# Performance work log

Measured on AMD Instinct MI355X. Metric: run time of the kernel, lower is better.

## Reference

```python
import jax, jax.numpy as jnp
import numpy as np

T, B, V, D, H = 1024, 128, 50257, 128, 512


def _lstm_cell(x, h, c, w_ih, w_hh, b_ih, b_hh):
    # x: [B, D], h/c: [B, H]; gates: [B, 4H] in PyTorch i,f,g,o order
    gates = x @ w_ih.T + h @ w_hh.T + b_ih + b_hh
    i, f, g, o = jnp.split(gates, 4, axis=-1)
    c_new = jax.nn.sigmoid(f) * c + jax.nn.sigmoid(i) * jnp.tanh(g)
    h_new = jax.nn.sigmoid(o) * jnp.tanh(c_new)
    return h_new, c_new


def setup_inputs() -> dict:
    key = jax.random.key(0)
    ks = jax.random.split(key, 7)
    s = 1.0 / np.sqrt(H)
    return {
        "input_ids": jax.random.randint(ks[0], (T, B), 0, V),
        "seq_len": jnp.sort(jax.random.randint(ks[1], (B,), 0, T)),
        "emb_weight": jax.random.normal(ks[2], (V, D), jnp.float32) * 0.1,
        "w_ih": jax.random.uniform(ks[3], (4 * H, D), jnp.float32, -s, s),
        "w_hh": jax.random.uniform(ks[4], (4 * H, H), jnp.float32, -s, s),
        "b_ih": jax.random.uniform(ks[5], (4 * H,), jnp.float32, -s, s),
        "b_hh": jax.random.uniform(ks[6], (4 * H,), jnp.float32, -s, s),
    }


def reference(input_ids, seq_len, emb_weight, w_ih, w_hh, b_ih, b_hh):
    Tn, Bn = input_ids.shape
    Hn = w_hh.shape[1]
    dt = emb_weight.dtype
    z = jnp.zeros((Bn, Hn), dt)

    def step(carry, inp):
        h, c, last_h, last_c = carry
        t, ids = inp
        x = emb_weight[ids]                       # embedding lookup (dropout=identity, eval)
        h_new, c_new = _lstm_cell(x, h, c, w_ih, w_hh, b_ih, b_hh)
        # hold previously reported features once timestep >= seq_len (skip blend at t==0)
        hold = ((t > 0) & (t >= seq_len)).astype(dt)[:, None]
        blend_c = c_new * (1.0 - hold) + last_c * hold
        blend_h = h_new * (1.0 - hold) + last_h * hold
        # RNN internal state keeps evolving (module is stateful across steps)
        return (h_new, c_new, blend_h, blend_c), None

    (_, _, _, final_c), _ = jax.lax.scan(
        step, (z, z, z, z), (jnp.arange(Tn), input_ids)
    )
    return final_c  # [B, H] mask-blended last cell state
```

## Files before the change

kernel.cpp:

```cpp
#include <hip/hip_runtime.h>

typedef _Float16 half8 __attribute__((ext_vector_type(8)));
typedef float float4v __attribute__((ext_vector_type(4)));
typedef unsigned long long u64;

#define TSEQ  1024
#define BATCH 128
#define HID   512
#define DIN   128

#define HW_STRIDE 264
#define HBUF_WORDS (8 * HW_STRIDE)
#define GOFF (2 * HBUF_WORDS * 4)
#define LDS_BYTES (GOFF + 4 * 8 * 32 * 4)

#define WS_H16_OFF  0
#define WS_BAR_OFF  (2 * BATCH * HID * 2)
#define WS_XALL_OFF (1u << 20)
#define WS_NEED     ((size_t)WS_XALL_OFF + (size_t)TSEQ * BATCH * DIN * 2)

__device__ inline half8 cvt8(float4v a, float4v b) {
    half8 r;
    r[0] = (_Float16)a[0]; r[1] = (_Float16)a[1];
    r[2] = (_Float16)a[2]; r[3] = (_Float16)a[3];
    r[4] = (_Float16)b[0]; r[5] = (_Float16)b[1];
    r[6] = (_Float16)b[2]; r[7] = (_Float16)b[3];
    return r;
}

__device__ inline float sigm(float x) {
    return __builtin_amdgcn_rcpf(1.0f + __builtin_amdgcn_exp2f(-1.44269504f * x));
}
__device__ inline float tanh_fast(float x) { return 2.0f * sigm(2.0f * x) - 1.0f; }

template <bool XA>
__global__ __launch_bounds__(256, 1)
void lstm_persistent(const int* __restrict__ ids,
                     const int* __restrict__ seq_len,
                     const float* __restrict__ emb,
                     const float* __restrict__ w_ih,
                     const float* __restrict__ w_hh,
                     const float* __restrict__ b_ih,
                     const float* __restrict__ b_hh,
                     float* __restrict__ out,
                     _Float16* __restrict__ h16,
                     _Float16* __restrict__ x_all,
                     int* __restrict__ bar)
{
    __shared__ __align__(16) char smem[LDS_BYTES];
    unsigned* hsu = (unsigned*)smem;
    _Float16* hsh = (_Float16*)smem;
    float*    gs  = (float*)(smem + GOFF);

    const int tid  = threadIdx.x;
    const int lane = tid & 63;
    const int wv   = tid >> 6;
    const int team = blockIdx.x & 15;
    const int p    = blockIdx.x >> 4;
    const int rowbase   = team * 8;
    const int unit_base = p * 32 + wv * 8;

    const int col  = lane & 15;
    const int kq   = lane >> 4;
    const int arow = lane & 7;
    const int my_row  = lane >> 3;
    const int my_unit = unit_base + (lane & 7);

    if (XA) {
        for (int pair = blockIdx.x * 256 + tid; pair < TSEQ * BATCH;
             pair += 256 * 256) {
            const float* src = emb + (size_t)ids[pair] * DIN;
            _Float16* dst = x_all + (size_t)pair * DIN;
#pragma unroll
            for (int k = 0; k < 16; ++k) {
                float4v a = *(const float4v*)(src + k * 8);
                float4v c = *(const float4v*)(src + k * 8 + 4);
                *(half8*)(dst + k * 8) = cvt8(a, c);
            }
        }
        __threadfence();
        __syncthreads();
        if (tid == 0) {
            __hip_atomic_fetch_add(bar, 1, __ATOMIC_RELEASE,
                                   __HIP_MEMORY_SCOPE_AGENT);
            int g = 0;
            while (__hip_atomic_load(bar, __ATOMIC_ACQUIRE,
                                     __HIP_MEMORY_SCOPE_AGENT) < 256
                   && ++g < (1 << 26)) { }
        }
        __syncthreads();
        __threadfence();
    }

    int tmax = 0, my_tstar = 0;
    for (int r = 0; r < 8; ++r) {
        int s  = seq_len[rowbase + r];
        int ts = (s > 0) ? (s - 1) : 0;
        if (r == my_row) my_tstar = ts;
        tmax = (ts > tmax) ? ts : tmax;
    }

    const int wrow0 = (col & 3) * HID + unit_base + (col >> 2);
    const int wrow1 = (col & 3) * HID + unit_base + 4 + (col >> 2);
    const float bias0 = b_ih[wrow0] + b_hh[wrow0];
    const float bias1 = b_ih[wrow1] + b_hh[wrow1];

    half8 whhf0[16], whhf1[16];
#pragma unroll
    for (int kt = 0; kt < 16; ++kt) {
        const float* s0 = w_hh + (size_t)wrow0 * HID + kt * 32 + kq * 8;
        const float* s1 = w_hh + (size_t)wrow1 * HID + kt * 32 + kq * 8;
        whhf0[kt] = cvt8(*(const float4v*)s0, *(const float4v*)(s0 + 4));
        whhf1[kt] = cvt8(*(const float4v*)s1, *(const float4v*)(s1 + 4));
    }
    half8 wihf0[4], wihf1[4];
#pragma unroll
    for (int kt = 0; kt < 4; ++kt) {
        const float* s0 = w_ih + (size_t)wrow0 * DIN + kt * 32 + kq * 8;
        const float* s1 = w_ih + (size_t)wrow1 * DIN + kt * 32 + kq * 8;
        wihf0[kt] = cvt8(*(const float4v*)s0, *(const float4v*)(s0 + 4));
        wihf1[kt] = cvt8(*(const float4v*)s1, *(const float4v*)(s1 + 4));
    }

    float c_state = 0.0f;
    const int crow = tid >> 5;
    const int coff = tid & 31;

    half8 xf[4], xn[4];
    if (XA) {
        const _Float16* x0 = x_all + ((size_t)0 * BATCH + rowbase + arow) * DIN;
        const int t1 = (tmax > 0) ? 1 : 0;
        const _Float16* x1 = x_all + ((size_t)t1 * BATCH + rowbase + arow) * DIN;
#pragma unroll
        for (int kt = 0; kt < 4; ++kt) {
            xf[kt] = *(const half8*)(x0 + kt * 32 + kq * 8);
            xn[kt] = *(const half8*)(x1 + kt * 32 + kq * 8);
        }
    } else {
        const int id0 = ids[rowbase + arow];
        const float* xrow = emb + (size_t)id0 * DIN;
#pragma unroll
        for (int kt = 0; kt < 4; ++kt) {
            const float* s = xrow + kt * 32 + kq * 8;
            xf[kt] = cvt8(*(const float4v*)s, *(const float4v*)(s + 4));
        }
    }

    float4v a0 = {bias0, bias0, bias0, bias0}, b0 = {0,0,0,0}, c0 = {0,0,0,0}, d0 = {0,0,0,0};
    float4v a1 = {bias1, bias1, bias1, bias1}, b1 = {0,0,0,0}, c1 = {0,0,0,0}, d1 = {0,0,0,0};
    a0 = __builtin_amdgcn_mfma_f32_16x16x32_f16(xf[0], wihf0[0], a0, 0, 0, 0);
    b0 = __builtin_amdgcn_mfma_f32_16x16x32_f16(xf[1], wihf0[1], b0, 0, 0, 0);
    c0 = __builtin_amdgcn_mfma_f32_16x16x32_f16(xf[2], wihf0[2], c0, 0, 0, 0);
    d0 = __builtin_amdgcn_mfma_f32_16x16x32_f16(xf[3], wihf0[3], d0, 0, 0, 0);
    a1 = __builtin_amdgcn_mfma_f32_16x16x32_f16(xf[0], wihf1[0], a1, 0, 0, 0);
    b1 = __builtin_amdgcn_mfma_f32_16x16x32_f16(xf[1], wihf1[1], b1, 0, 0, 0);
    c1 = __builtin_amdgcn_mfma_f32_16x16x32_f16(xf[2], wihf1[2], c1, 0, 0, 0);
    d1 = __builtin_amdgcn_mfma_f32_16x16x32_f16(xf[3], wihf1[3], d1, 0, 0, 0);

    const u64 LSBM = 0x0001000100010001ull;

    for (int t = 0; t <= tmax; ++t) {
        const int bs = t & 1;
        int id_next = 0;
        if (!XA) {
            const int tn = (t < tmax) ? (t + 1) : t;
            id_next = ids[tn * BATCH + rowbase + arow];
        }

        if (t > 0) {
            const u64* rowp = (const u64*)(h16
                + (size_t)((t + 1) & 1) * BATCH * HID + (rowbase + crow) * HID);
            const u64 want = ((((t - 1) >> 1) & 1) ^ 1) ? LSBM : 0ull;
            unsigned* dstw = hsu + bs * HBUF_WORDS + crow * HW_STRIDE + 2 * coff;
            u64 v[4];
            unsigned pending = 0xF;
#pragma unroll
            for (int j = 0; j < 4; ++j)
                v[j] = __hip_atomic_load(rowp + coff + 32 * j,
                                         __ATOMIC_RELAXED, __HIP_MEMORY_SCOPE_AGENT);
#pragma unroll
            for (int j = 0; j < 4; ++j) {
                if (((v[j] ^ want) & LSBM) == 0) {
                    *(u64*)(dstw + 64 * j) = v[j];
                    pending &= ~(1u << j);
                }
            }
            int round = 0, guard = 0;
            while (pending) {
#pragma unroll
                for (int j = 0; j < 4; ++j) {
                    if (pending & (1u << j)) {
                        u64 x = __hip_atomic_load(rowp + coff + 32 * j,
                                                  __ATOMIC_RELAXED,
                                                  __HIP_MEMORY_SCOPE_AGENT);
                        if (((x ^ want) & LSBM) == 0) {
                            *(u64*)(dstw + 64 * j) = x;
                            pending &= ~(1u << j);
                        }
                    }
                }
                if (!pending) break;
                if (++round >= 3) __builtin_amdgcn_s_sleep(1);
                if (++guard > (1 << 20)) break;
            }
        }
        __syncthreads();

        float4v xraw[8];
        if (!XA) {
            const float* xrow = emb + (size_t)id_next * DIN;
#pragma unroll
            for (int kt = 0; kt < 4; ++kt) {
                xraw[2 * kt]     = *(const float4v*)(xrow + kt * 32 + kq * 8);
                xraw[2 * kt + 1] = *(const float4v*)(xrow + kt * 32 + kq * 8 + 4);
            }
        }

        if (t > 0) {
            const _Float16* hb = hsh + bs * HBUF_WORDS * 2;
#pragma unroll
            for (int kt = 0; kt < 16; ++kt) {
                half8 af = *(const half8*)(hb + arow * (HW_STRIDE * 2) + kt * 32 + kq * 8);
                switch (kt & 3) {
                case 0:
                    a0 = __builtin_amdgcn_mfma_f32_16x16x32_f16(af, whhf0[kt], a0, 0, 0, 0);
                    a1 = __builtin_amdgcn_mfma_f32_16x16x32_f16(af, whhf1[kt], a1, 0, 0, 0);
                    break;
                case 1:
                    b0 = __builtin_amdgcn_mfma_f32_16x16x32_f16(af, whhf0[kt], b0, 0, 0, 0);
                    b1 = __builtin_amdgcn_mfma_f32_16x16x32_f16(af, whhf1[kt], b1, 0, 0, 0);
                    break;
                case 2:
                    c0 = __builtin_amdgcn_mfma_f32_16x16x32_f16(af, whhf0[kt], c0, 0, 0, 0);
                    c1 = __builtin_amdgcn_mfma_f32_16x16x32_f16(af, whhf1[kt], c1, 0, 0, 0);
                    break;
                default:
                    d0 = __builtin_amdgcn_mfma_f32_16x16x32_f16(af, whhf0[kt], d0, 0, 0, 0);
                    d1 = __builtin_amdgcn_mfma_f32_16x16x32_f16(af, whhf1[kt], d1, 0, 0, 0);
                }
            }
        }
        const float4v g0 = (a0 + b0) + (c0 + d0);
        const float4v g1 = (a1 + b1) + (c1 + d1);

        float* gw = gs + wv * 256;
        if (lane < 32) {
            const int grow = (lane >> 4) * 4;
#pragma unroll
            for (int r = 0; r < 4; ++r) {
                gw[(grow + r) * 32 + col]      = g0[r];
                gw[(grow + r) * 32 + 16 + col] = g1[r];
            }
        }
        const float4v g4 = *(const float4v*)(gw + my_row * 32 + (lane & 7) * 4);

        const float i_s = sigm(g4[0]);
        const float f_s = sigm(g4[1]);
        const float g_t = tanh_fast(g4[2]);
        const float o_s = sigm(g4[3]);
        c_state = f_s * c_state + i_s * g_t;
        const float hn = o_s * tanh_fast(c_state);

        if (t == my_tstar)
            out[(rowbase + my_row) * HID + my_unit] = c_state;

        {
            const unsigned pub_phase = (((unsigned)t >> 1) & 1u) ^ 1u;
            unsigned short hb16 = __builtin_bit_cast(unsigned short, (_Float16)hn);
            hb16 = (unsigned short)((hb16 & 0xFFFEu) | pub_phase);
            __hip_atomic_store((unsigned short*)h16
                                   + (size_t)(t & 1) * BATCH * HID
                                   + (rowbase + my_row) * HID + my_unit,
                               hb16, __ATOMIC_RELAXED, __HIP_MEMORY_SCOPE_AGENT);
        }

        if (XA) {
#pragma unroll
            for (int kt = 0; kt < 4; ++kt) xf[kt] = xn[kt];
            const int t2 = (t + 2 <= tmax) ? (t + 2) : tmax;
            const _Float16* xs2 = x_all + ((size_t)t2 * BATCH + rowbase + arow) * DIN;
#pragma unroll
            for (int kt = 0; kt < 4; ++kt)
                xn[kt] = *(const half8*)(xs2 + kt * 32 + kq * 8);
        } else {
#pragma unroll
            for (int kt = 0; kt < 4; ++kt)
                xf[kt] = cvt8(xraw[2 * kt], xraw[2 * kt + 1]);
        }

        a0 = (float4v){bias0, bias0, bias0, bias0}; b0 = (float4v){0,0,0,0};
        c0 = (float4v){0,0,0,0};                    d0 = (float4v){0,0,0,0};
        a1 = (float4v){bias1, bias1, bias1, bias1}; b1 = (float4v){0,0,0,0};
        c1 = (float4v){0,0,0,0};                    d1 = (float4v){0,0,0,0};
        a0 = __builtin_amdgcn_mfma_f32_16x16x32_f16(xf[0], wihf0[0], a0, 0, 0, 0);
        b0 = __builtin_amdgcn_mfma_f32_16x16x32_f16(xf[1], wihf0[1], b0, 0, 0, 0);
        c0 = __builtin_amdgcn_mfma_f32_16x16x32_f16(xf[2], wihf0[2], c0, 0, 0, 0);
        d0 = __builtin_amdgcn_mfma_f32_16x16x32_f16(xf[3], wihf0[3], d0, 0, 0, 0);
        a1 = __builtin_amdgcn_mfma_f32_16x16x32_f16(xf[0], wihf1[0], a1, 0, 0, 0);
        b1 = __builtin_amdgcn_mfma_f32_16x16x32_f16(xf[1], wihf1[1], b1, 0, 0, 0);
        c1 = __builtin_amdgcn_mfma_f32_16x16x32_f16(xf[2], wihf1[2], c1, 0, 0, 0);
        d1 = __builtin_amdgcn_mfma_f32_16x16x32_f16(xf[3], wihf1[3], d1, 0, 0, 0);
    }
}

extern "C" void kernel_launch(void* const* d_in, const int* in_sizes, int n_in,
                              void* d_out, int out_size, void* d_ws, size_t ws_size,
                              hipStream_t stream)
{
    const int*   ids  = (const int*)d_in[0];
    const int*   slen = (const int*)d_in[1];
    const float* emb  = (const float*)d_in[2];
    const float* wih  = (const float*)d_in[3];
    const float* whh  = (const float*)d_in[4];
    const float* bih  = (const float*)d_in[5];
    const float* bhh  = (const float*)d_in[6];
    float* out = (float*)d_out;

    _Float16* h16   = (_Float16*)((char*)d_ws + WS_H16_OFF);
    int*      bar   = (int*)((char*)d_ws + WS_BAR_OFF);
    _Float16* x_all = (_Float16*)((char*)d_ws + WS_XALL_OFF);

    if (ws_size >= WS_NEED) {
        hipMemsetAsync(bar, 0, sizeof(int), stream);
        hipLaunchKernelGGL((lstm_persistent<true>), dim3(256), dim3(256), 0, stream,
                           ids, slen, emb, wih, whh, bih, bhh, out,
                           h16, x_all, bar);
    } else {
        hipLaunchKernelGGL((lstm_persistent<false>), dim3(256), dim3(256), 0, stream,
                           ids, slen, emb, wih, whh, bih, bhh, out,
                           h16, x_all, bar);
    }
}
```

Measured before the change: 2.064 ms.

## Use XCC-local sc0 polling for h exchange when a team shares one XCC

At the global barrier each block records its XCC id, and every team checks whether all 16 of its blocks sit on the same XCC. If they do, the recurrent h polling uses sc0 loads (served at the XCC-shared L2 level, bypassing L1) for the first rounds. It falls back to agent-scope atomic loads if sc0 polling keeps failing. When the team is co-located, h is also published with an extra workgroup-scope store, to cut cross-die coherence latency in the per-step exchange. This relies on undocumented block placement and adds inline asm and a duplicate store per step; the sleep threshold and guard limit also change.

Measured after the change: 5.475 ms. 2.65x slower.

```diff
diff --git a/kernel.cpp b/kernel.cpp
--- a/kernel.cpp
+++ b/kernel.cpp
@@ -32,6 +32,30 @@
     return __builtin_amdgcn_rcpf(1.0f + __builtin_amdgcn_exp2f(-1.44269504f * x));
 }
 __device__ inline float tanh_fast(float x) { return 2.0f * sigm(2.0f * x) - 1.0f; }
+
+__device__ inline int get_xcc_id() {
+    int x;
+    asm volatile("s_getreg_b32 %0, hwreg(HW_REG_XCC_ID)" : "=s"(x));
+    return x;
+}
+
+__device__ inline void ld4_sc0(const u64* p, u64* v) {
+    asm volatile(
+        "global_load_dwordx2 %0, %4, off sc0\n\t"
+        "global_load_dwordx2 %1, %4, off offset:256 sc0\n\t"
+        "global_load_dwordx2 %2, %4, off offset:512 sc0\n\t"
+        "global_load_dwordx2 %3, %4, off offset:768 sc0\n\t"
+        "s_waitcnt vmcnt(0)"
+        : "=&v"(v[0]), "=&v"(v[1]), "=&v"(v[2]), "=&v"(v[3])
+        : "v"(p) : "memory");
+}
+__device__ inline u64 ld1_sc0(const u64* p) {
+    u64 v;
+    asm volatile("global_load_dwordx2 %0, %1, off sc0\n\t"
+                 "s_waitcnt vmcnt(0)"
+                 : "=&v"(v) : "v"(p) : "memory");
+    return v;
+}
 
 template <bool XA>
 __global__ __launch_bounds__(256, 1)
@@ -48,6 +72,7 @@
                      int* __restrict__ bar)
 {
     __shared__ __align__(16) char smem[LDS_BYTES];
+    __shared__ int fastflag;
     unsigned* hsu = (unsigned*)smem;
     _Float16* hsh = (_Float16*)smem;
     float*    gs  = (float*)(smem + GOFF);
@@ -78,6 +103,7 @@
                 *(half8*)(dst + k * 8) = cvt8(a, c);
             }
         }
+        if (tid == 0) bar[1 + blockIdx.x] = get_xcc_id() + 1;
         __threadfence();
         __syncthreads();
         if (tid == 0) {
@@ -90,7 +116,20 @@
         }
         __syncthreads();
         __threadfence();
-    }
+        if (tid == 0) {
+            const int mine = get_xcc_id() + 1;
+            int f = 1;
+            for (int pp = 0; pp < 16; ++pp) {
+                int xv = __hip_atomic_load(bar + 1 + (16 * pp + team),
+                                           __ATOMIC_RELAXED,
+                                           __HIP_MEMORY_SCOPE_AGENT);
+                f &= (xv == mine);
+            }
+            fastflag = f;
+        }
+        __syncthreads();
+    }
+    const int fast = XA ? fastflag : 0;
 
     int tmax = 0, my_tstar = 0;
     for (int r = 0; r < 8; ++r) {
@@ -159,6 +198,9 @@
 
     const u64 LSBM = 0x0001000100010001ull;
 
+    int use_sc0 = fast;
+    int sc0_credit = 4;
+
     for (int t = 0; t <= tmax; ++t) {
         const int bs = t & 1;
         int id_next = 0;
@@ -174,10 +216,16 @@
             unsigned* dstw = hsu + bs * HBUF_WORDS + crow * HW_STRIDE + 2 * coff;
             u64 v[4];
             unsigned pending = 0xF;
-#pragma unroll
-            for (int j = 0; j < 4; ++j)
-                v[j] = __hip_atomic_load(rowp + coff + 32 * j,
-                                         __ATOMIC_RELAXED, __HIP_MEMORY_SCOPE_AGENT);
+            const int sc0r = use_sc0 ? 4 : 0;
+            if (sc0r) {
+                ld4_sc0(rowp + coff, v);
+            } else {
+#pragma unroll
+                for (int j = 0; j < 4; ++j)
+                    v[j] = __hip_atomic_load(rowp + coff + 32 * j,
+                                             __ATOMIC_RELAXED,
+                                             __HIP_MEMORY_SCOPE_AGENT);
+            }
 #pragma unroll
             for (int j = 0; j < 4; ++j) {
                 if (((v[j] ^ want) & LSBM) == 0) {
@@ -185,23 +233,33 @@
                     pending &= ~(1u << j);
                 }
             }
-            int round = 0, guard = 0;
+            unsigned sc0_sat = sc0r ? (~pending & 0xFu) : 0u;
+            int round = 1, guard = 0;
+            const int sleep_thr = sc0r + 3;
             while (pending) {
 #pragma unroll
                 for (int j = 0; j < 4; ++j) {
                     if (pending & (1u << j)) {
-                        u64 x = __hip_atomic_load(rowp + coff + 32 * j,
-                                                  __ATOMIC_RELAXED,
-                                                  __HIP_MEMORY_SCOPE_AGENT);
+                        u64 x = (round <= sc0r)
+                                  ? ld1_sc0(rowp + coff + 32 * j)
+                                  : __hip_atomic_load(rowp + coff + 32 * j,
+                                                      __ATOMIC_RELAXED,
+                                                      __HIP_MEMORY_SCOPE_AGENT);
                         if (((x ^ want) & LSBM) == 0) {
                             *(u64*)(dstw + 64 * j) = x;
                             pending &= ~(1u << j);
+                            if (round <= sc0r) sc0_sat |= (1u << j);
                         }
                     }
                 }
                 if (!pending) break;
-                if (++round >= 3) __builtin_amdgcn_s_sleep(1);
-                if (++guard > (1 << 20)) break;
+                if (round >= sleep_thr) __builtin_amdgcn_s_sleep(1);
+                ++round;
+                if (++guard > (1 << 18)) break;
+            }
+            if (sc0r) {
+                if (sc0_sat) sc0_credit = 4;
+                else if (--sc0_credit <= 0) use_sc0 = 0;
             }
         }
         __syncthreads();
@@ -268,10 +326,14 @@
             const unsigned pub_phase = (((unsigned)t >> 1) & 1u) ^ 1u;
             unsigned short hb16 = __builtin_bit_cast(unsigned short, (_Float16)hn);
             hb16 = (unsigned short)((hb16 & 0xFFFEu) | pub_phase);
-            __hip_atomic_store((unsigned short*)h16
-                                   + (size_t)(t & 1) * BATCH * HID
-                                   + (rowbase + my_row) * HID + my_unit,
-                               hb16, __ATOMIC_RELAXED, __HIP_MEMORY_SCOPE_AGENT);
+            unsigned short* hdst = (unsigned short*)h16
+                + (size_t)(t & 1) * BATCH * HID
+                + (rowbase + my_row) * HID + my_unit;
+            if (fast)
+                __hip_atomic_store(hdst, hb16, __ATOMIC_RELAXED,
+                                   __HIP_MEMORY_SCOPE_WORKGROUP);
+            __hip_atomic_store(hdst, hb16, __ATOMIC_RELAXED,
+                               __HIP_MEMORY_SCOPE_AGENT);
         }
 
         if (XA) {
```

## Process two batch row-groups per block with interleaved half-steps, halving grid size

Applied to the files above, without the earlier changes.

Each persistent block now handles two 8-row batch groups (A and B) instead of one, with 128 blocks instead of 256. Within each timestep the block polls and computes group A, then polls and computes group B, so one group's cross-block h exchange can overlap the other's compute. Weights held in registers are reused across both groups. The cost is twice the serial work per block per step, more registers and LDS, and a tmax taken over 16 rows instead of 8.

After: 3.534 ms. +71.2%, slower.

```diff
diff --git a/kernel.cpp b/kernel.cpp
--- a/kernel.cpp
+++ b/kernel.cpp
@@ -11,7 +11,7 @@
 
 #define HW_STRIDE 264
 #define HBUF_WORDS (8 * HW_STRIDE)
-#define GOFF (2 * HBUF_WORDS * 4)
+#define GOFF (4 * HBUF_WORDS * 4)
 #define LDS_BYTES (GOFF + 4 * 8 * 32 * 4)
 
 #define WS_H16_OFF  0
@@ -55,9 +55,10 @@
     const int tid  = threadIdx.x;
     const int lane = tid & 63;
     const int wv   = tid >> 6;
-    const int team = blockIdx.x & 15;
-    const int p    = blockIdx.x >> 4;
-    const int rowbase   = team * 8;
+    const int pairk = blockIdx.x & 7;
+    const int p     = blockIdx.x >> 3;
+    const int rowbaseA = pairk * 16;
+    const int rowbaseB = pairk * 16 + 8;
     const int unit_base = p * 32 + wv * 8;
 
     const int col  = lane & 15;
@@ -67,10 +68,10 @@
     const int my_unit = unit_base + (lane & 7);
 
     if (XA) {
-        for (int pair = blockIdx.x * 256 + tid; pair < TSEQ * BATCH;
-             pair += 256 * 256) {
-            const float* src = emb + (size_t)ids[pair] * DIN;
-            _Float16* dst = x_all + (size_t)pair * DIN;
+        for (int pr = blockIdx.x * 256 + tid; pr < TSEQ * BATCH;
+             pr += 128 * 256) {
+            const float* src = emb + (size_t)ids[pr] * DIN;
+            _Float16* dst = x_all + (size_t)pr * DIN;
 #pragma unroll
             for (int k = 0; k < 16; ++k) {
                 float4v a = *(const float4v*)(src + k * 8);
@@ -85,18 +86,19 @@
                                    __HIP_MEMORY_SCOPE_AGENT);
             int g = 0;
             while (__hip_atomic_load(bar, __ATOMIC_ACQUIRE,
-                                     __HIP_MEMORY_SCOPE_AGENT) < 256
+                                     __HIP_MEMORY_SCOPE_AGENT) < (int)gridDim.x
                    && ++g < (1 << 26)) { }
         }
         __syncthreads();
         __threadfence();
     }
 
-    int tmax = 0, my_tstar = 0;
-    for (int r = 0; r < 8; ++r) {
-        int s  = seq_len[rowbase + r];
+    int tmax = 0, my_tstarA = 0, my_tstarB = 0;
+    for (int r = 0; r < 16; ++r) {
+        int s  = seq_len[pairk * 16 + r];
         int ts = (s > 0) ? (s - 1) : 0;
-        if (r == my_row) my_tstar = ts;
+        if (r == my_row)     my_tstarA = ts;
+        if (r == 8 + my_row) my_tstarB = ts;
         tmax = (ts > tmax) ? ts : tmax;
     }
 
@@ -122,55 +124,75 @@
         wihf1[kt] = cvt8(*(const float4v*)s1, *(const float4v*)(s1 + 4));
     }
 
-    float c_state = 0.0f;
+    float cA = 0.0f, cB = 0.0f;
     const int crow = tid >> 5;
     const int coff = tid & 31;
 
-    half8 xf[4], xn[4];
+    half8 xfA[4], xnA[4], xfB[4], xnB[4];
     if (XA) {
-        const _Float16* x0 = x_all + ((size_t)0 * BATCH + rowbase + arow) * DIN;
         const int t1 = (tmax > 0) ? 1 : 0;
-        const _Float16* x1 = x_all + ((size_t)t1 * BATCH + rowbase + arow) * DIN;
+        const _Float16* a0p = x_all + ((size_t)0 * BATCH + rowbaseA + arow) * DIN;
+        const _Float16* a1p = x_all + ((size_t)t1 * BATCH + rowbaseA + arow) * DIN;
+        const _Float16* b0p = x_all + ((size_t)0 * BATCH + rowbaseB + arow) * DIN;
+        const _Float16* b1p = x_all + ((size_t)t1 * BATCH + rowbaseB + arow) * DIN;
 #pragma unroll
         for (int kt = 0; kt < 4; ++kt) {
-            xf[kt] = *(const half8*)(x0 + kt * 32 + kq * 8);
-            xn[kt] = *(const half8*)(x1 + kt * 32 + kq * 8);
+            xfA[kt] = *(const half8*)(a0p + kt * 32 + kq * 8);
+            xnA[kt] = *(const half8*)(a1p + kt * 32 + kq * 8);
+            xfB[kt] = *(const half8*)(b0p + kt * 32 + kq * 8);
+            xnB[kt] = *(const half8*)(b1p + kt * 32 + kq * 8);
         }
     } else {
-        const int id0 = ids[rowbase + arow];
-        const float* xrow = emb + (size_t)id0 * DIN;
+        const int idA = ids[rowbaseA + arow];
+        const int idB = ids[rowbaseB + arow];
+        const float* xa = emb + (size_t)idA * DIN;
+        const float* xb = emb + (size_t)idB * DIN;
 #pragma unroll
         for (int kt = 0; kt < 4; ++kt) {
-            const float* s = xrow + kt * 32 + kq * 8;
-            xf[kt] = cvt8(*(const float4v*)s, *(const float4v*)(s + 4));
-        }
-    }
-
-    float4v a0 = {bias0, bias0, bias0, bias0}, b0 = {0,0,0,0}, c0 = {0,0,0,0}, d0 = {0,0,0,0};
-    float4v a1 = {bias1, bias1, bias1, bias1}, b1 = {0,0,0,0}, c1 = {0,0,0,0}, d1 = {0,0,0,0};
-    a0 = __builtin_amdgcn_mfma_f32_16x16x32_f16(xf[0], wihf0[0], a0, 0, 0, 0);
-    b0 = __builtin_amdgcn_mfma_f32_16x16x32_f16(xf[1], wihf0[1], b0, 0, 0, 0);
-    c0 = __builtin_amdgcn_mfma_f32_16x16x32_f16(xf[2], wihf0[2], c0, 0, 0, 0);
-    d0 = __builtin_amdgcn_mfma_f32_16x16x32_f16(xf[3], wihf0[3], d0, 0, 0, 0);
-    a1 = __builtin_amdgcn_mfma_f32_16x16x32_f16(xf[0], wihf1[0], a1, 0, 0, 0);
-    b1 = __builtin_amdgcn_mfma_f32_16x16x32_f16(xf[1], wihf1[1], b1, 0, 0, 0);
-    c1 = __builtin_amdgcn_mfma_f32_16x16x32_f16(xf[2], wihf1[2], c1, 0, 0, 0);
-    d1 = __builtin_amdgcn_mfma_f32_16x16x32_f16(xf[3], wihf1[3], d1, 0, 0, 0);
+            const float* sa = xa + kt * 32 + kq * 8;
+            const float* sb = xb + kt * 32 + kq * 8;
+            xfA[kt] = cvt8(*(const float4v*)sa, *(const float4v*)(sa + 4));
+            xfB[kt] = cvt8(*(const float4v*)sb, *(const float4v*)(sb + 4));
+        }
+    }
+
+    float4v Aa0 = {bias0, bias0, bias0, bias0}, Ab0 = {0,0,0,0}, Ac0 = {0,0,0,0}, Ad0 = {0,0,0,0};
+    float4v Aa1 = {bias1, bias1, bias1, bias1}, Ab1 = {0,0,0,0}, Ac1 = {0,0,0,0}, Ad1 = {0,0,0,0};
+    float4v Ba0 = {bias0, bias0, bias0, bias0}, Bb0 = {0,0,0,0}, Bc0 = {0,0,0,0}, Bd0 = {0,0,0,0};
+    float4v Ba1 = {bias1, bias1, bias1, bias1}, Bb1 = {0,0,0,0}, Bc1 = {0,0,0,0}, Bd1 = {0,0,0,0};
+    Aa0 = __builtin_amdgcn_mfma_f32_16x16x32_f16(xfA[0], wihf0[0], Aa0, 0, 0, 0);
+    Ab0 = __builtin_amdgcn_mfma_f32_16x16x32_f16(xfA[1], wihf0[1], Ab0, 0, 0, 0);
+    Ac0 = __builtin_amdgcn_mfma_f32_16x16x32_f16(xfA[2], wihf0[2], Ac0, 0, 0, 0);
+    Ad0 = __builtin_amdgcn_mfma_f32_16x16x32_f16(xfA[3], wihf0[3], Ad0, 0, 0, 0);
+    Aa1 = __builtin_amdgcn_mfma_f32_16x16x32_f16(xfA[0], wihf1[0], Aa1, 0, 0, 0);
+    Ab1 = __builtin_amdgcn_mfma_f32_16x16x32_f16(xfA[1], wihf1[1], Ab1, 0, 0, 0);
+    Ac1 = __builtin_amdgcn_mfma_f32_16x16x32_f16(xfA[2], wihf1[2], Ac1, 0, 0, 0);
+    Ad1 = __builtin_amdgcn_mfma_f32_16x16x32_f16(xfA[3], wihf1[3], Ad1, 0, 0, 0);
+    Ba0 = __builtin_amdgcn_mfma_f32_16x16x32_f16(xfB[0], wihf0[0], Ba0, 0, 0, 0);
+    Bb0 = __builtin_amdgcn_mfma_f32_16x16x32_f16(xfB[1], wihf0[1], Bb0, 0, 0, 0);
+    Bc0 = __builtin_amdgcn_mfma_f32_16x16x32_f16(xfB[2], wihf0[2], Bc0, 0, 0, 0);
+    Bd0 = __builtin_amdgcn_mfma_f32_16x16x32_f16(xfB[3], wihf0[3], Bd0, 0, 0, 0);
+    Ba1 = __builtin_amdgcn_mfma_f32_16x16x32_f16(xfB[0], wihf1[0], Ba1, 0, 0, 0);
+    Bb1 = __builtin_amdgcn_mfma_f32_16x16x32_f16(xfB[1], wihf1[1], Bb1, 0, 0, 0);
+    Bc1 = __builtin_amdgcn_mfma_f32_16x16x32_f16(xfB[2], wihf1[2], Bc1, 0, 0, 0);
+    Bd1 = __builtin_amdgcn_mfma_f32_16x16x32_f16(xfB[3], wihf1[3], Bd1, 0, 0, 0);
 
     const u64 LSBM = 0x0001000100010001ull;
 
     for (int t = 0; t <= tmax; ++t) {
         const int bs = t & 1;
-        int id_next = 0;
+        const u64 want = ((((t - 1) >> 1) & 1) ^ 1) ? LSBM : 0ull;
+        const unsigned pub_phase = (((unsigned)t >> 1) & 1u) ^ 1u;
+        const size_t pub_base = (size_t)(t & 1) * BATCH * HID;
+        const size_t pol_base = (size_t)((t + 1) & 1) * BATCH * HID;
+
+        int id_nextA = 0;
         if (!XA) {
             const int tn = (t < tmax) ? (t + 1) : t;
-            id_next = ids[tn * BATCH + rowbase + arow];
-        }
-
+            id_nextA = ids[tn * BATCH + rowbaseA + arow];
+        }
         if (t > 0) {
-            const u64* rowp = (const u64*)(h16
-                + (size_t)((t + 1) & 1) * BATCH * HID + (rowbase + crow) * HID);
-            const u64 want = ((((t - 1) >> 1) & 1) ^ 1) ? LSBM : 0ull;
+            const u64* rowp = (const u64*)(h16 + pol_base + (rowbaseA + crow) * HID);
             unsigned* dstw = hsu + bs * HBUF_WORDS + crow * HW_STRIDE + 2 * coff;
             u64 v[4];
             unsigned pending = 0xF;
@@ -206,13 +228,13 @@
         }
         __syncthreads();
 
-        float4v xraw[8];
+        float4v xrawA[8];
         if (!XA) {
-            const float* xrow = emb + (size_t)id_next * DIN;
+            const float* xrow = emb + (size_t)id_nextA * DIN;
 #pragma unroll
             for (int kt = 0; kt < 4; ++kt) {
-                xraw[2 * kt]     = *(const float4v*)(xrow + kt * 32 + kq * 8);
-                xraw[2 * kt + 1] = *(const float4v*)(xrow + kt * 32 + kq * 8 + 4);
+                xrawA[2 * kt]     = *(const float4v*)(xrow + kt * 32 + kq * 8);
+                xrawA[2 * kt + 1] = *(const float4v*)(xrow + kt * 32 + kq * 8 + 4);
             }
         }
 
@@ -223,83 +245,204 @@
                 half8 af = *(const half8*)(hb + arow * (HW_STRIDE * 2) + kt * 32 + kq * 8);
                 switch (kt & 3) {
                 case 0:
-                    a0 = __builtin_amdgcn_mfma_f32_16x16x32_f16(af, whhf0[kt], a0, 0, 0, 0);
-                    a1 = __builtin_amdgcn_mfma_f32_16x16x32_f16(af, whhf1[kt], a1, 0, 0, 0);
+                    Aa0 = __builtin_amdgcn_mfma_f32_16x16x32_f16(af, whhf0[kt], Aa0, 0, 0, 0);
+                    Aa1 = __builtin_amdgcn_mfma_f32_16x16x32_f16(af, whhf1[kt], Aa1, 0, 0, 0);
                     break;
                 case 1:
-                    b0 = __builtin_amdgcn_mfma_f32_16x16x32_f16(af, whhf0[kt], b0, 0, 0, 0);
-                    b1 = __builtin_amdgcn_mfma_f32_16x16x32_f16(af, whhf1[kt], b1, 0, 0, 0);
+                    Ab0 = __builtin_amdgcn_mfma_f32_16x16x32_f16(af, whhf0[kt], Ab0, 0, 0, 0);
+                    Ab1 = __builtin_amdgcn_mfma_f32_16x16x32_f16(af, whhf1[kt], Ab1, 0, 0, 0);
                     break;
                 case 2:
-                    c0 = __builtin_amdgcn_mfma_f32_16x16x32_f16(af, whhf0[kt], c0, 0, 0, 0);
-                    c1 = __builtin_amdgcn_mfma_f32_16x16x32_f16(af, whhf1[kt], c1, 0, 0, 0);
+                    Ac0 = __builtin_amdgcn_mfma_f32_16x16x32_f16(af, whhf0[kt], Ac0, 0, 0, 0);
+                    Ac1 = __builtin_amdgcn_mfma_f32_16x16x32_f16(af, whhf1[kt], Ac1, 0, 0, 0);
                     break;
                 default:
-                    d0 = __builtin_amdgcn_mfma_f32_16x16x32_f16(af, whhf0[kt], d0, 0, 0, 0);
-                    d1 = __builtin_amdgcn_mfma_f32_16x16x32_f16(af, whhf1[kt], d1, 0, 0, 0);
-                }
-            }
-        }
-        const float4v g0 = (a0 + b0) + (c0 + d0);
-        const float4v g1 = (a1 + b1) + (c1 + d1);
-
-        float* gw = gs + wv * 256;
-        if (lane < 32) {
-            const int grow = (lane >> 4) * 4;
-#pragma unroll
-            for (int r = 0; r < 4; ++r) {
-                gw[(grow + r) * 32 + col]      = g0[r];
-                gw[(grow + r) * 32 + 16 + col] = g1[r];
-            }
-        }
-        const float4v g4 = *(const float4v*)(gw + my_row * 32 + (lane & 7) * 4);
-
-        const float i_s = sigm(g4[0]);
-        const float f_s = sigm(g4[1]);
-        const float g_t = tanh_fast(g4[2]);
-        const float o_s = sigm(g4[3]);
-        c_state = f_s * c_state + i_s * g_t;
-        const float hn = o_s * tanh_fast(c_state);
-
-        if (t == my_tstar)
-            out[(rowbase + my_row) * HID + my_unit] = c_state;
-
+                    Ad0 = __builtin_amdgcn_mfma_f32_16x16x32_f16(af, whhf0[kt], Ad0, 0, 0, 0);
+                    Ad1 = __builtin_amdgcn_mfma_f32_16x16x32_f16(af, whhf1[kt], Ad1, 0, 0, 0);
+                }
+            }
+        }
         {
-            const unsigned pub_phase = (((unsigned)t >> 1) & 1u) ^ 1u;
+            const float4v g0 = (Aa0 + Ab0) + (Ac0 + Ad0);
+            const float4v g1 = (Aa1 + Ab1) + (Ac1 + Ad1);
+            float* gw = gs + wv * 256;
+            if (lane < 32) {
+                const int grow = (lane >> 4) * 4;
+#pragma unroll
+                for (int r = 0; r < 4; ++r) {
+                    gw[(grow + r) * 32 + col]      = g0[r];
+                    gw[(grow + r) * 32 + 16 + col] = g1[r];
+                }
+            }
+            const float4v g4 = *(const float4v*)(gw + my_row * 32 + (lane & 7) * 4);
+            const float i_s = sigm(g4[0]);
+            const float f_s = sigm(g4[1]);
+            const float g_t = tanh_fast(g4[2]);
+            const float o_s = sigm(g4[3]);
+            cA = f_s * cA + i_s * g_t;
+            const float hn = o_s * tanh_fast(cA);
+            if (t == my_tstarA)
+                out[(rowbaseA + my_row) * HID + my_unit] = cA;
             unsigned short hb16 = __builtin_bit_cast(unsigned short, (_Float16)hn);
             hb16 = (unsigned short)((hb16 & 0xFFFEu) | pub_phase);
-            __hip_atomic_store((unsigned short*)h16
-                                   + (size_t)(t & 1) * BATCH * HID
-                                   + (rowbase + my_row) * HID + my_unit,
+            __hip_atomic_store((unsigned short*)h16 + pub_base
+                                   + (rowbaseA + my_row) * HID + my_unit,
                                hb16, __ATOMIC_RELAXED, __HIP_MEMORY_SCOPE_AGENT);
         }
-
         if (XA) {
 #pragma unroll
-            for (int kt = 0; kt < 4; ++kt) xf[kt] = xn[kt];
+            for (int kt = 0; kt < 4; ++kt) xfA[kt] = xnA[kt];
             const int t2 = (t + 2 <= tmax) ? (t + 2) : tmax;
-            const _Float16* xs2 = x_all + ((size_t)t2 * BATCH + rowbase + arow) * DIN;
+            const _Float16* xs2 = x_all + ((size_t)t2 * BATCH + rowbaseA + arow) * DIN;
 #pragma unroll
             for (int kt = 0; kt < 4; ++kt)
-                xn[kt] = *(const half8*)(xs2 + kt * 32 + kq * 8);
+                xnA[kt] = *(const half8*)(xs2 + kt * 32 + kq * 8);
         } else {
 #pragma unroll
             for (int kt = 0; kt < 4; ++kt)
-                xf[kt] = cvt8(xraw[2 * kt], xraw[2 * kt + 1]);
-        }
-
-        a0 = (float4v){bias0, bias0, bias0, bias0}; b0 = (float4v){0,0,0,0};
-        c0 = (float4v){0,0,0,0};                    d0 = (float4v){0,0,0,0};
-        a1 = (float4v){bias1, bias1, bias1, bias1}; b1 = (float4v){0,0,0,0};
-        c1 = (float4v){0,0,0,0};                    d1 = (float4v){0,0,0,0};
-        a0 = __builtin_amdgcn_mfma_f32_16x16x32_f16(xf[0], wihf0[0], a0, 0, 0, 0);
-        b0 = __builtin_amdgcn_mfma_f32_16x16x32_f16(xf[1], wihf0[1], b0, 0, 0, 0);
-        c0 = __builtin_amdgcn_mfma_f32_16x16x32_f16(xf[2], wihf0[2], c0, 0, 0, 0);
-        d0 = __builtin_amdgcn_mfma_f32_16x16x32_f16(xf[3], wihf0[3], d0, 0, 0, 0);
-        a1 = __builtin_amdgcn_mfma_f32_16x16x32_f16(xf[0], wihf1[0], a1, 0, 0, 0);
-        b1 = __builtin_amdgcn_mfma_f32_16x16x32_f16(xf[1], wihf1[1], b1, 0, 0, 0);
-        c1 = __builtin_amdgcn_mfma_f32_16x16x32_f16(xf[2], wihf1[2], c1, 0, 0, 0);
-        d1 = __builtin_amdgcn_mfma_f32_16x16x32_f16(xf[3], wihf1[3], d1, 0, 0, 0);
+                xfA[kt] = cvt8(xrawA[2 * kt], xrawA[2 * kt + 1]);
+        }
+        Aa0 = (float4v){bias0, bias0, bias0, bias0}; Ab0 = (float4v){0,0,0,0};
+        Ac0 = (float4v){0,0,0,0};                    Ad0 = (float4v){0,0,0,0};
+        Aa1 = (float4v){bias1, bias1, bias1, bias1}; Ab1 = (float4v){0,0,0,0};
+        Ac1 = (float4v){0,0,0,0};                    Ad1 = (float4v){0,0,0,0};
+        Aa0 = __builtin_amdgcn_mfma_f32_16x16x32_f16(xfA[0], wihf0[0], Aa0, 0, 0, 0);
+        Ab0 = __builtin_amdgcn_mfma_f32_16x16x32_f16(xfA[1], wihf0[1], Ab0, 0, 0, 0);
+        Ac0 = __builtin_amdgcn_mfma_f32_16x16x32_f16(xfA[2], wihf0[2], Ac0, 0, 0, 0);
+        Ad0 = __builtin_amdgcn_mfma_f32_16x16x32_f16(xfA[3], wihf0[3], Ad0, 0, 0, 0);
+        Aa1 = __builtin_amdgcn_mfma_f32_16x16x32_f16(xfA[0], wihf1[0], Aa1, 0, 0, 0);
+        Ab1 = __builtin_amdgcn_mfma_f32_16x16x32_f16(xfA[1], wihf1[1], Ab1, 0, 0, 0);
+        Ac1 = __builtin_amdgcn_mfma_f32_16x16x32_f16(xfA[2], wihf1[2], Ac1, 0, 0, 0);
+        Ad1 = __builtin_amdgcn_mfma_f32_16x16x32_f16(xfA[3], wihf1[3], Ad1, 0, 0, 0);
+
+        int id_nextB = 0;
+        if (!XA) {
+            const int tn = (t < tmax) ? (t + 1) : t;
+            id_nextB = ids[tn * BATCH + rowbaseB + arow];
+        }
+        if (t > 0) {
+            const u64* rowp = (const u64*)(h16 + pol_base + (rowbaseB + crow) * HID);
+            unsigned* dstw = hsu + (2 + bs) * HBUF_WORDS + crow * HW_STRIDE + 2 * coff;
+            u64 v[4];
+            unsigned pending = 0xF;
+#pragma unroll
+            for (int j = 0; j < 4; ++j)
+                v[j] = __hip_atomic_load(rowp + coff + 32 * j,
+                                         __ATOMIC_RELAXED, __HIP_MEMORY_SCOPE_AGENT);
+#pragma unroll
+            for (int j = 0; j < 4; ++j) {
+                if (((v[j] ^ want) & LSBM) == 0) {
+                    *(u64*)(dstw + 64 * j) = v[j];
+                    pending &= ~(1u << j);
+                }
+            }
+            int round = 0, guard = 0;
+            while (pending) {
+#pragma unroll
+                for (int j = 0; j < 4; ++j) {
+                    if (pending & (1u << j)) {
+                        u64 x = __hip_atomic_load(rowp + coff + 32 * j,
+                                                  __ATOMIC_RELAXED,
+                                                  __HIP_MEMORY_SCOPE_AGENT);
+                        if (((x ^ want) & LSBM) == 0) {
+                            *(u64*)(dstw + 64 * j) = x;
+                            pending &= ~(1u << j);
+                        }
+                    }
+                }
+                if (!pending) break;
+                if (++round >= 3) __builtin_amdgcn_s_sleep(1);
+                if (++guard > (1 << 20)) break;
+            }
+        }
+        __syncthreads();
+
+        float4v xrawB[8];
+        if (!XA) {
+            const float* xrow = emb + (size_t)id_nextB * DIN;
+#pragma unroll
+            for (int kt = 0; kt < 4; ++kt) {
+                xrawB[2 * kt]     = *(const float4v*)(xrow + kt * 32 + kq * 8);
+                xrawB[2 * kt + 1] = *(const float4v*)(xrow + kt * 32 + kq * 8 + 4);
+            }
+        }
+
+        if (t > 0) {
+            const _Float16* hb = hsh + (2 + bs) * HBUF_WORDS * 2;
+#pragma unroll
+            for (int kt = 0; kt < 16; ++kt) {
+                half8 af = *(const half8*)(hb + arow * (HW_STRIDE * 2) + kt * 32 + kq * 8);
+                switch (kt & 3) {
+                case 0:
+                    Ba0 = __builtin_amdgcn_mfma_f32_16x16x32_f16(af, whhf0[kt], Ba0, 0, 0, 0);
+                    Ba1 = __builtin_amdgcn_mfma_f32_16x16x32_f16(af, whhf1[kt], Ba1, 0, 0, 0);
+                    break;
+                case 1:
+                    Bb0 = __builtin_amdgcn_mfma_f32_16x16x32_f16(af, whhf0[kt], Bb0, 0, 0, 0);
+                    Bb1 = __builtin_amdgcn_mfma_f32_16x16x32_f16(af, whhf1[kt], Bb1, 0, 0, 0);
+                    break;
+                case 2:
+                    Bc0 = __builtin_amdgcn_mfma_f32_16x16x32_f16(af, whhf0[kt], Bc0, 0, 0, 0);
+                    Bc1 = __builtin_amdgcn_mfma_f32_16x16x32_f16(af, whhf1[kt], Bc1, 0, 0, 0);
+                    break;
+                default:
+                    Bd0 = __builtin_amdgcn_mfma_f32_16x16x32_f16(af, whhf0[kt], Bd0, 0, 0, 0);
+                    Bd1 = __builtin_amdgcn_mfma_f32_16x16x32_f16(af, whhf1[kt], Bd1, 0, 0, 0);
+                }
+            }
+        }
+        {
+            const float4v g0 = (Ba0 + Bb0) + (Bc0 + Bd0);
+            const float4v g1 = (Ba1 + Bb1) + (Bc1 + Bd1);
+            float* gw = gs + wv * 256;
+            if (lane < 32) {
+                const int grow = (lane >> 4) * 4;
+#pragma unroll
+                for (int r = 0; r < 4; ++r) {
+                    gw[(grow + r) * 32 + col]      = g0[r];
+                    gw[(grow + r) * 32 + 16 + col] = g1[r];
+                }
+            }
+            const float4v g4 = *(const float4v*)(gw + my_row * 32 + (lane & 7) * 4);
+            const float i_s = sigm(g4[0]);
+            const float f_s = sigm(g4[1]);
+            const float g_t = tanh_fast(g4[2]);
+            const float o_s = sigm(g4[3]);
+            cB = f_s * cB + i_s * g_t;
+            const float hn = o_s * tanh_fast(cB);
+            if (t == my_tstarB)
+                out[(rowbaseB + my_row) * HID + my_unit] = cB;
+            unsigned short hb16 = __builtin_bit_cast(unsigned short, (_Float16)hn);
+            hb16 = (unsigned short)((hb16 & 0xFFFEu) | pub_phase);
+            __hip_atomic_store((unsigned short*)h16 + pub_base
+                                   + (rowbaseB + my_row) * HID + my_unit,
+                               hb16, __ATOMIC_RELAXED, __HIP_MEMORY_SCOPE_AGENT);
+        }
+        if (XA) {
+#pragma unroll
+            for (int kt = 0; kt < 4; ++kt) xfB[kt] = xnB[kt];
+            const int t2 = (t + 2 <= tmax) ? (t + 2) : tmax;
+            const _Float16* xs2 = x_all + ((size_t)t2 * BATCH + rowbaseB + arow) * DIN;
+#pragma unroll
+            for (int kt = 0; kt < 4; ++kt)
+                xnB[kt] = *(const half8*)(xs2 + kt * 32 + kq * 8);
+        } else {
+#pragma unroll
+            for (int kt = 0; kt < 4; ++kt)
+                xfB[kt] = cvt8(xrawB[2 * kt], xrawB[2 * kt + 1]);
+        }
+        Ba0 = (float4v){bias0, bias0, bias0, bias0}; Bb0 = (float4v){0,0,0,0};
+        Bc0 = (float4v){0,0,0,0};                    Bd0 = (float4v){0,0,0,0};
+        Ba1 = (float4v){bias1, bias1, bias1, bias1}; Bb1 = (float4v){0,0,0,0};
+        Bc1 = (float4v){0,0,0,0};                    Bd1 = (float4v){0,0,0,0};
+        Ba0 = __builtin_amdgcn_mfma_f32_16x16x32_f16(xfB[0], wihf0[0], Ba0, 0, 0, 0);
+        Bb0 = __builtin_amdgcn_mfma_f32_16x16x32_f16(xfB[1], wihf0[1], Bb0, 0, 0, 0);
+        Bc0 = __builtin_amdgcn_mfma_f32_16x16x32_f16(xfB[2], wihf0[2], Bc0, 0, 0, 0);
+        Bd0 = __builtin_amdgcn_mfma_f32_16x16x32_f16(xfB[3], wihf0[3], Bd0, 0, 0, 0);
+        Ba1 = __builtin_amdgcn_mfma_f32_16x16x32_f16(xfB[0], wihf1[0], Ba1, 0, 0, 0);
+        Bb1 = __builtin_amdgcn_mfma_f32_16x16x32_f16(xfB[1], wihf1[1], Bb1, 0, 0, 0);
+        Bc1 = __builtin_amdgcn_mfma_f32_16x16x32_f16(xfB[2], wihf1[2], Bc1, 0, 0, 0);
+        Bd1 = __builtin_amdgcn_mfma_f32_16x16x32_f16(xfB[3], wihf1[3], Bd1, 0, 0, 0);
     }
 }
 
@@ -322,11 +465,11 @@
 
     if (ws_size >= WS_NEED) {
         hipMemsetAsync(bar, 0, sizeof(int), stream);
-        hipLaunchKernelGGL((lstm_persistent<true>), dim3(256), dim3(256), 0, stream,
+        hipLaunchKernelGGL((lstm_persistent<true>), dim3(128), dim3(256), 0, stream,
                            ids, slen, emb, wih, whh, bih, bhh, out,
                            h16, x_all, bar);
     } else {
-        hipLaunchKernelGGL((lstm_persistent<false>), dim3(256), dim3(256), 0, stream,
+        hipLaunchKernelGGL((lstm_persistent<false>), dim3(128), dim3(256), 0, stream,
                            ids, slen, emb, wih, whh, bih, bhh, out,
                            h16, x_all, bar);
     }
```

## Load recurrent h fragments straight from global into MFMA operands, drop LDS staging

Applied to the files above, without the earlier changes.

Each wave now polls the shared h16 buffer with relaxed atomic loads directly in the MFMA A-fragment layout. This removes the LDS staging buffer and the block-wide __syncthreads that previously sat between polling and the recurrent matmul. Loads for the 16 K-tiles are grouped into four batches and double-buffered so polling of later groups overlaps MFMAs on earlier ones. An adaptive sleep count before polling, raised on misses and lowered on hits, is meant to cut spin traffic on the coherence path, at the risk of adding latency when it overshoots.

New measurement: 7.375 ms. 3.57x slower.

```diff
diff --git a/kernel.cpp b/kernel.cpp
--- a/kernel.cpp
+++ b/kernel.cpp
@@ -9,15 +9,14 @@
 #define HID   512
 #define DIN   128
 
-#define HW_STRIDE 264
-#define HBUF_WORDS (8 * HW_STRIDE)
-#define GOFF (2 * HBUF_WORDS * 4)
-#define LDS_BYTES (GOFF + 4 * 8 * 32 * 4)
+#define LDS_BYTES (4 * 8 * 32 * 4)
 
 #define WS_H16_OFF  0
 #define WS_BAR_OFF  (2 * BATCH * HID * 2)
 #define WS_XALL_OFF (1u << 20)
 #define WS_NEED     ((size_t)WS_XALL_OFF + (size_t)TSEQ * BATCH * DIN * 2)
+
+struct U2 { u64 a, b; };
 
 __device__ inline half8 cvt8(float4v a, float4v b) {
     half8 r;
@@ -32,6 +31,8 @@
     return __builtin_amdgcn_rcpf(1.0f + __builtin_amdgcn_exp2f(-1.44269504f * x));
 }
 __device__ inline float tanh_fast(float x) { return 2.0f * sigm(2.0f * x) - 1.0f; }
+
+#define MF(A, B, C) __builtin_amdgcn_mfma_f32_16x16x32_f16((A), (B), (C), 0, 0, 0)
 
 template <bool XA>
 __global__ __launch_bounds__(256, 1)
@@ -47,10 +48,7 @@
                      _Float16* __restrict__ x_all,
                      int* __restrict__ bar)
 {
-    __shared__ __align__(16) char smem[LDS_BYTES];
-    unsigned* hsu = (unsigned*)smem;
-    _Float16* hsh = (_Float16*)smem;
-    float*    gs  = (float*)(smem + GOFF);
+    __shared__ __align__(16) float gs[4 * 8 * 32];
 
     const int tid  = threadIdx.x;
     const int lane = tid & 63;
@@ -123,8 +121,6 @@
     }
 
     float c_state = 0.0f;
-    const int crow = tid >> 5;
-    const int coff = tid & 31;
 
     half8 xf[4], xn[4];
     if (XA) {
@@ -148,64 +144,64 @@
 
     float4v a0 = {bias0, bias0, bias0, bias0}, b0 = {0,0,0,0}, c0 = {0,0,0,0}, d0 = {0,0,0,0};
     float4v a1 = {bias1, bias1, bias1, bias1}, b1 = {0,0,0,0}, c1 = {0,0,0,0}, d1 = {0,0,0,0};
-    a0 = __builtin_amdgcn_mfma_f32_16x16x32_f16(xf[0], wihf0[0], a0, 0, 0, 0);
-    b0 = __builtin_amdgcn_mfma_f32_16x16x32_f16(xf[1], wihf0[1], b0, 0, 0, 0);
-    c0 = __builtin_amdgcn_mfma_f32_16x16x32_f16(xf[2], wihf0[2], c0, 0, 0, 0);
-    d0 = __builtin_amdgcn_mfma_f32_16x16x32_f16(xf[3], wihf0[3], d0, 0, 0, 0);
-    a1 = __builtin_amdgcn_mfma_f32_16x16x32_f16(xf[0], wihf1[0], a1, 0, 0, 0);
-    b1 = __builtin_amdgcn_mfma_f32_16x16x32_f16(xf[1], wihf1[1], b1, 0, 0, 0);
-    c1 = __builtin_amdgcn_mfma_f32_16x16x32_f16(xf[2], wihf1[2], c1, 0, 0, 0);
-    d1 = __builtin_amdgcn_mfma_f32_16x16x32_f16(xf[3], wihf1[3], d1, 0, 0, 0);
+    a0 = MF(xf[0], wihf0[0], a0);  b0 = MF(xf[1], wihf0[1], b0);
+    c0 = MF(xf[2], wihf0[2], c0);  d0 = MF(xf[3], wihf0[3], d0);
+    a1 = MF(xf[0], wihf1[0], a1);  b1 = MF(xf[1], wihf1[1], b1);
+    c1 = MF(xf[2], wihf1[2], c1);  d1 = MF(xf[3], wihf1[3], d1);
 
     const u64 LSBM = 0x0001000100010001ull;
+    int slp = 6;
+
+#define AL8(idx) __hip_atomic_load(hp + (idx), __ATOMIC_RELAXED, \
+                                   __HIP_MEMORY_SCOPE_AGENT)
+#define LDG(buf, g) \
+    _Pragma("unroll") \
+    for (int k2 = 0; k2 < 4; ++k2) { \
+        buf[2*k2]   = AL8(((g)*4 + k2)*8 + ko); \
+        buf[2*k2+1] = AL8(((g)*4 + k2)*8 + ko + 1); \
+    }
+#define PROC(buf, g) { \
+    unsigned st = 0; \
+    _Pragma("unroll") \
+    for (int k2 = 0; k2 < 4; ++k2) \
+        if ((((buf[2*k2] ^ want) | (buf[2*k2+1] ^ want)) & LSBM) != 0) \
+            st |= 1u << k2; \
+    if ((g) == 0) miss0 = st; \
+    int round_ = 0, guard_ = 0; \
+    while (__any((int)st)) { \
+        _Pragma("unroll") \
+        for (int k2 = 0; k2 < 4; ++k2) { \
+            if (st & (1u << k2)) { \
+                u64 lo_ = AL8(((g)*4 + k2)*8 + ko); \
+                u64 hi_ = AL8(((g)*4 + k2)*8 + ko + 1); \
+                if ((((lo_ ^ want) | (hi_ ^ want)) & LSBM) == 0) { \
+                    buf[2*k2] = lo_; buf[2*k2+1] = hi_; st &= ~(1u << k2); \
+                } \
+            } \
+        } \
+        if (++round_ >= 3) __builtin_amdgcn_s_sleep(1); \
+        if (++guard_ > (1 << 20)) break; \
+    } \
+    _Pragma("unroll") \
+    for (int k2 = 0; k2 < 4; ++k2) { \
+        const int kt = (g)*4 + k2; \
+        U2 u2_; u2_.a = buf[2*k2]; u2_.b = buf[2*k2+1]; \
+        const half8 af = __builtin_bit_cast(half8, u2_); \
+        switch (k2) { \
+        case 0: a0 = MF(af, whhf0[kt], a0); a1 = MF(af, whhf1[kt], a1); break; \
+        case 1: b0 = MF(af, whhf0[kt], b0); b1 = MF(af, whhf1[kt], b1); break; \
+        case 2: c0 = MF(af, whhf0[kt], c0); c1 = MF(af, whhf1[kt], c1); break; \
+        default: d0 = MF(af, whhf0[kt], d0); d1 = MF(af, whhf1[kt], d1); \
+        } \
+    } }
 
     for (int t = 0; t <= tmax; ++t) {
-        const int bs = t & 1;
         int id_next = 0;
         if (!XA) {
             const int tn = (t < tmax) ? (t + 1) : t;
             id_next = ids[tn * BATCH + rowbase + arow];
         }
 
-        if (t > 0) {
-            const u64* rowp = (const u64*)(h16
-                + (size_t)((t + 1) & 1) * BATCH * HID + (rowbase + crow) * HID);
-            const u64 want = ((((t - 1) >> 1) & 1) ^ 1) ? LSBM : 0ull;
-            unsigned* dstw = hsu + bs * HBUF_WORDS + crow * HW_STRIDE + 2 * coff;
-            u64 v[4];
-            unsigned pending = 0xF;
-#pragma unroll
-            for (int j = 0; j < 4; ++j)
-                v[j] = __hip_atomic_load(rowp + coff + 32 * j,
-                                         __ATOMIC_RELAXED, __HIP_MEMORY_SCOPE_AGENT);
-#pragma unroll
-            for (int j = 0; j < 4; ++j) {
-                if (((v[j] ^ want) & LSBM) == 0) {
-                    *(u64*)(dstw + 64 * j) = v[j];
-                    pending &= ~(1u << j);
-                }
-            }
-            int round = 0, guard = 0;
-            while (pending) {
-#pragma unroll
-                for (int j = 0; j < 4; ++j) {
-                    if (pending & (1u << j)) {
-                        u64 x = __hip_atomic_load(rowp + coff + 32 * j,
-                                                  __ATOMIC_RELAXED,
-                                                  __HIP_MEMORY_SCOPE_AGENT);
-                        if (((x ^ want) & LSBM) == 0) {
-                            *(u64*)(dstw + 64 * j) = x;
-                            pending &= ~(1u << j);
-                        }
-                    }
-                }
-                if (!pending) break;
-                if (++round >= 3) __builtin_amdgcn_s_sleep(1);
-                if (++guard > (1 << 20)) break;
-            }
-        }
-        __syncthreads();
-
         float4v xraw[8];
         if (!XA) {
             const float* xrow = emb + (size_t)id_next * DIN;
@@ -217,29 +213,27 @@
         }
 
         if (t > 0) {
-            const _Float16* hb = hsh + bs * HBUF_WORDS * 2;
-#pragma unroll
-            for (int kt = 0; kt < 16; ++kt) {
-                half8 af = *(const half8*)(hb + arow * (HW_STRIDE * 2) + kt * 32 + kq * 8);
-                switch (kt & 3) {
-                case 0:
-                    a0 = __builtin_amdgcn_mfma_f32_16x16x32_f16(af, whhf0[kt], a0, 0, 0, 0);
-                    a1 = __builtin_amdgcn_mfma_f32_16x16x32_f16(af, whhf1[kt], a1, 0, 0, 0);
-                    break;
-                case 1:
-                    b0 = __builtin_amdgcn_mfma_f32_16x16x32_f16(af, whhf0[kt], b0, 0, 0, 0);
-                    b1 = __builtin_amdgcn_mfma_f32_16x16x32_f16(af, whhf1[kt], b1, 0, 0, 0);
-                    break;
-                case 2:
-                    c0 = __builtin_amdgcn_mfma_f32_16x16x32_f16(af, whhf0[kt], c0, 0, 0, 0);
-                    c1 = __builtin_amdgcn_mfma_f32_16x16x32_f16(af, whhf1[kt], c1, 0, 0, 0);
-                    break;
-                default:
-                    d0 = __builtin_amdgcn_mfma_f32_16x16x32_f16(af, whhf0[kt], d0, 0, 0, 0);
-                    d1 = __builtin_amdgcn_mfma_f32_16x16x32_f16(af, whhf1[kt], d1, 0, 0, 0);
-                }
-            }
-        }
+            for (int i = 0; i < slp; ++i) __builtin_amdgcn_s_sleep(1);
+
+            const u64* hp = (const u64*)(h16
+                + (size_t)((t + 1) & 1) * BATCH * HID + (rowbase + arow) * HID);
+            const int ko = kq * 2;
+            const u64 want = ((((t - 1) >> 1) & 1) ^ 1) ? LSBM : 0ull;
+            unsigned miss0 = 0;
+            u64 L0[8], L1[8];
+            LDG(L0, 0);
+            LDG(L1, 1);
+            PROC(L0, 0);
+            LDG(L0, 2);
+            PROC(L1, 1);
+            LDG(L1, 3);
+            PROC(L0, 2);
+            PROC(L1, 3);
+
+            if (__any((int)miss0)) slp = (slp < 24) ? slp + 1 : 24;
+            else                   slp = (slp > 1)  ? slp - 1 : 1;
+        }
+
         const float4v g0 = (a0 + b0) + (c0 + d0);
         const float4v g1 = (a1 + b1) + (c1 + d1);
 
@@ -292,15 +286,14 @@
         c0 = (float4v){0,0,0,0};                    d0 = (float4v){0,0,0,0};
         a1 = (float4v){bias1, bias1, bias1, bias1}; b1 = (float4v){0,0,0,0};
         c1 = (float4v){0,0,0,0};                    d1 = (float4v){0,0,0,0};
-        a0 = __builtin_amdgcn_mfma_f32_16x16x32_f16(xf[0], wihf0[0], a0, 0, 0, 0);
-        b0 = __builtin_amdgcn_mfma_f32_16x16x32_f16(xf[1], wihf0[1], b0, 0, 0, 0);
-        c0 = __builtin_amdgcn_mfma_f32_16x16x32_f16(xf[2], wihf0[2], c0, 0, 0, 0);
-        d0 = __builtin_amdgcn_mfma_f32_16x16x32_f16(xf[3], wihf0[3], d0, 0, 0, 0);
-        a1 = __builtin_amdgcn_mfma_f32_16x16x32_f16(xf[0], wihf1[0], a1, 0, 0, 0);
-        b1 = __builtin_amdgcn_mfma_f32_16x16x32_f16(xf[1], wihf1[1], b1, 0, 0, 0);
-        c1 = __builtin_amdgcn_mfma_f32_16x16x32_f16(xf[2], wihf1[2], c1, 0, 0, 0);
-        d1 = __builtin_amdgcn_mfma_f32_16x16x32_f16(xf[3], wihf1[3], d1, 0, 0, 0);
-    }
+        a0 = MF(xf[0], wihf0[0], a0);  b0 = MF(xf[1], wihf0[1], b0);
+        c0 = MF(xf[2], wihf0[2], c0);  d0 = MF(xf[3], wihf0[3], d0);
+        a1 = MF(xf[0], wihf1[0], a1);  b1 = MF(xf[1], wihf1[1], b1);
+        c1 = MF(xf[2], wihf1[2], c1);  d1 = MF(xf[3], wihf1[3], d1);
+    }
+#undef AL8
+#undef LDG
+#undef PROC
 }
 
 extern "C" void kernel_launch(void* const* d_in, const int* in_sizes, int n_in,
```
